# Optimization experiments

Hardware: AMD Instinct MI355X
Metric: run time of the kernel (lower is better)

## Reference

```python
import jax, jax.numpy as jnp
import numpy as np

B, N, D = 8, 256, 128


def setup_inputs() -> dict:
    key = jax.random.key(0)
    ks = jax.random.split(key, 4)
    s1 = 1.0 / np.sqrt(4 * D)
    s2 = 1.0 / np.sqrt(2 * D)
    s3 = 1.0 / np.sqrt(D)
    return {
        "tour_features": jax.random.normal(ks[0], (B, N, D), dtype=jnp.float32),
        "W1": jax.random.uniform(ks[1], (4 * D, 2 * D), jnp.float32, -s1, s1),
        "b1": jnp.zeros((2 * D,), jnp.float32),
        "W2": jax.random.uniform(ks[2], (2 * D, D), jnp.float32, -s2, s2),
        "b2": jnp.zeros((D,), jnp.float32),
        "W3": jax.random.uniform(ks[3], (D, 1), jnp.float32, -s3, s3),
        "b3": jnp.zeros((1,), jnp.float32),
    }


def reference(tour_features, W1, b1, W2, b2, W3, b3):
    Bs, Ns, Ds = tour_features.shape
    x = tour_features
    x_next = jnp.roll(x, -1, axis=1)  # node at (k+1) % N
    # Split first linear's weight by the 4 concatenated feature blocks:
    # cat([x_i, x_{i+1}, x_j, x_{j+1}]) @ W1 == x_i@W1a + x_{i+1}@W1b + x_j@W1c + x_{j+1}@W1d
    W1a, W1b, W1c, W1d = jnp.split(W1, 4, axis=0)
    Pi = x @ W1a + x_next @ W1b          # [B, N, 2D] (i-side projection)
    Pj = x @ W1c + x_next @ W1d          # [B, N, 2D] (j-side projection)
    h1 = jax.nn.relu(Pi[:, :, None, :] + Pj[:, None, :, :] + b1)  # [B, N, N, 2D]
    h2 = jax.nn.relu(h1 @ W2 + b2)       # [B, N, N, D]
    score = jnp.tanh((h2 @ W3 + b3)[..., 0])  # [B, N, N]
    # Valid pairs: j >= i + 2 and not (j - i == N - 1)
    ii = jnp.arange(Ns)[:, None]
    jj = jnp.arange(Ns)[None, :]
    mask = (jj >= ii + 2) & (jj - ii != Ns - 1)
    improvement_matrix = jnp.where(mask[None], score, 0.0)
    improved_tour = jnp.broadcast_to(jnp.arange(Ns), (Bs, Ns))
    return improved_tour, improvement_matrix
```

## Files before the change

### kernel.cpp

```cpp
#include <hip/hip_runtime.h>


typedef __attribute__((ext_vector_type(8))) short short8;
typedef __attribute__((ext_vector_type(8))) _Float16 half8;
typedef __attribute__((ext_vector_type(4))) float floatx4;

static __device__ __forceinline__ unsigned short f2bf(float f) {
  unsigned int x = __float_as_uint(f);
  x += 0x7fff + ((x >> 16) & 1);
  return (unsigned short)(x >> 16);
}

static __device__ __forceinline__ unsigned short f2h(float f) {
  _Float16 h = (_Float16)f;
  return __builtin_bit_cast(unsigned short, h);
}

static __device__ __forceinline__ float fast_tanh(float x) {
  float e = __expf(2.0f * fabsf(x));
  float t = 1.0f - 2.0f * __builtin_amdgcn_rcpf(e + 1.0f);
  return copysignf(t, x);
}

static __device__ __forceinline__ long pack_fp8(half8 s) {
  int lo = __builtin_amdgcn_cvt_pk_fp8_f32((float)s[0], (float)s[1], 0, false);
  lo = __builtin_amdgcn_cvt_pk_fp8_f32((float)s[2], (float)s[3], lo, true);
  int hi = __builtin_amdgcn_cvt_pk_fp8_f32((float)s[4], (float)s[5], 0, false);
  hi = __builtin_amdgcn_cvt_pk_fp8_f32((float)s[6], (float)s[7], hi, true);
  return (long)(unsigned)lo | ((long)hi << 32);
}

static __device__ __forceinline__ void gload_lds16(const void* g, void* l) {
  __builtin_amdgcn_global_load_lds(
      (const __attribute__((address_space(1))) unsigned int*)g,
      (__attribute__((address_space(3))) unsigned int*)l, 16, 0, 0);
}

__global__ __launch_bounds__(256) void k_prep(
    const float* __restrict__ x, const float* __restrict__ W1,
    const float* __restrict__ W2, float* __restrict__ out,
    unsigned char* __restrict__ W2F8, unsigned short* __restrict__ W1T,
    unsigned short* __restrict__ xcat) {
  int e = blockIdx.x * 256 + threadIdx.x;
  if (e < 2048) {
    out[e] = (float)(e & 255);
  } else if (e < 526336) {
    out[e] = 0.f;
  } else if (e < 542720) {
    int t = e - 526336;
    int p = t >> 7, n = t & 127;
    float f0 = W2[(2 * p) * 128 + n] * 16.f;
    float f1 = W2[(2 * p + 1) * 128 + n] * 16.f;
    int v2 = __builtin_amdgcn_cvt_pk_fp8_f32(f0, f1, 0, false);
    int q = n >> 5, which = (n >> 4) & 1, l = n & 15;
    int c = p >> 2, off = (p & 3) * 2;
    int cs = (c & 16) | ((c ^ l) & 15);
    *(unsigned short*)(W2F8 + q * 8192 + l * 512 + cs * 16 + which * 8 + off) =
        (unsigned short)(v2 & 0xffff);
  } else if (e < 673792) {
    int e3 = e - 542720;
    int n = e3 >> 8, k = e3 & 255;
    int v = k >> 3;
    int sw = (((v & 16) | ((v ^ (n & 15)) & 15)) << 3) | (k & 7);
    W1T[(n << 8) + sw] = f2bf(W1[((k + (n & 256)) << 8) + (n & 255)]);
  } else {
    int e4 = e - 673792;
    int r = e4 >> 8, k = e4 & 255;
    int v = k >> 3;
    int sw = (((v & 16) | ((v ^ (r & 15)) & 15)) << 3) | (k & 7);
    int pos = r & 255;
    int pos2 = (k < 128) ? pos : ((pos + 1) & 255);
    xcat[(r << 8) + sw] = f2bf(x[(((r >> 8) << 8) + pos2) * 128 + (k & 127)]);
  }
}

__global__ __launch_bounds__(256) void k_proj(
    const unsigned short* __restrict__ xcat, const unsigned short* __restrict__ W1T,
    const float* __restrict__ b1, unsigned short* __restrict__ PiH,
    unsigned short* __restrict__ PjH) {
  const int mg = blockIdx.x >> 3;
  const int ng = blockIdx.x & 7;
  const int tid = threadIdx.x;
  const int wr = tid >> 6, lane = tid & 63, quad = lane >> 4, l15 = lane & 15;

  __shared__ unsigned short As[64 * 256];
  __shared__ unsigned short Bs[64 * 256];

  const unsigned short* Asrc = xcat + mg * 64 * 256;
  const unsigned short* Bsrc = W1T + ng * 64 * 256;
#pragma unroll
  for (int it = 0; it < 8; ++it) {
    const int c = it * 256 + wr * 64 + lane;
    gload_lds16(Asrc + c * 8, &As[(it * 256 + wr * 64) * 8]);
    gload_lds16(Bsrc + c * 8, &Bs[(it * 256 + wr * 64) * 8]);
  }
  __syncthreads();

  floatx4 acc[4];
#pragma unroll
  for (int mt = 0; mt < 4; ++mt) acc[mt] = (floatx4)0.f;

  const char* Ab = (const char*)As;
  const char* Bb = (const char*)Bs + wr * 16 * 512;
  const int base_sw = l15 * 512 + ((quad ^ l15) << 4);

#pragma unroll
  for (int ks = 0; ks < 8; ++ks) {
    const int swz = base_sw ^ (ks << 6);
    short8 bfr = *(const short8*)(Bb + swz);
#pragma unroll
    for (int mt = 0; mt < 4; ++mt) {
      short8 afr = *(const short8*)(Ab + mt * 8192 + swz);
      acc[mt] = __builtin_amdgcn_mfma_f32_16x16x32_bf16(afr, bfr, acc[mt], 0, 0, 0);
    }
  }

  const int ch = ng * 64 + wr * 16 + l15;
  const float bias = (ch < 256) ? b1[ch] : 0.f;
  const bool isPi = (ch < 256);
  unsigned short* dst = isPi ? PiH : PjH;
  const int chan = ch & 255;
  const int ck = chan >> 3, coff = chan & 7;
#pragma unroll
  for (int mt = 0; mt < 4; ++mt)
#pragma unroll
    for (int r = 0; r < 4; ++r) {
      int row = mg * 64 + mt * 16 + quad * 4 + r;
      int cpos;
      if (isPi) cpos = chan;
      else {
        int cs = (ck & 16) | ((ck ^ (row & 15)) & 15);
        cpos = cs * 8 + coff;
      }
      dst[row * 256 + cpos] = f2h(acc[mt][r] + bias);
    }
}

__global__ __launch_bounds__(256, 3) void k_main(
    const unsigned short* __restrict__ PiH, const unsigned short* __restrict__ PjH,
    const unsigned char* __restrict__ W2F8, const float* __restrict__ b2,
    const float* __restrict__ W3, const float* __restrict__ b3,
    float* __restrict__ outm) {
  const int tid = threadIdx.x;
  const int wr = tid >> 6;
  const int lane = tid & 63, quad = lane >> 4, l15 = lane & 15;

  __shared__ unsigned char W2s[32768];
  __shared__ unsigned char PjS[16384];
  __shared__ unsigned char PiS[4096];

  const int bid = blockIdx.x;
  const int b = bid / 288;
  const int rem = bid - b * 288;
  int jt = 0, basej = 0;
  if (rem >= 8)   { jt = 1; basej = 8;   }
  if (rem >= 24)  { jt = 2; basej = 24;  }
  if (rem >= 48)  { jt = 3; basej = 48;  }
  if (rem >= 80)  { jt = 4; basej = 80;  }
  if (rem >= 120) { jt = 5; basej = 120; }
  if (rem >= 168) { jt = 6; basej = 168; }
  if (rem >= 224) { jt = 7; basej = 224; }
  const int i = (rem - basej) * 4 + wr;

  const unsigned char* pjsrc =
      (const unsigned char*)(PjH + ((b << 8) + jt * 32) * 256);
  const unsigned char* pisrc =
      (const unsigned char*)(PiH + ((b << 8) + i) * 256);
#pragma unroll
  for (int it = 0; it < 8; ++it) {
    const int c = it * 256 + wr * 64 + lane;
    gload_lds16(W2F8 + c * 16, &W2s[(it * 256 + wr * 64) * 16]);
  }
#pragma unroll
  for (int it = 0; it < 4; ++it) {
    const int c = it * 256 + wr * 64 + lane;
    gload_lds16(pjsrc + c * 16, &PjS[(it * 256 + wr * 64) * 16]);
  }
  gload_lds16(pisrc + (lane & 31) * 16, &PiS[wr * 1024]);
  __syncthreads();

  const char* W2base = (const char*)&W2s[0];
  const char* PjBase = (const char*)&PjS[0];
  const char* PiBase = (const char*)&PiS[0] + wr * 1024 + quad * 16;
  const int sw16 = l15 * 512 + (((quad ^ l15) & 15) << 4);

  floatx4 acc[2][8];
#pragma unroll
  for (int mt = 0; mt < 2; ++mt)
#pragma unroll
    for (int nt = 0; nt < 8; ++nt) acc[mt][nt] = (floatx4)0.f;

  union U4 { uint4 v; half8 h; };
  U4 piR[2], pjR[2][2];
  piR[0].v = *(const uint4*)(PiBase);
  pjR[0][0].v = *(const uint4*)(PjBase + sw16);
  pjR[0][1].v = *(const uint4*)(PjBase + 8192 + sw16);
  piR[1].v = *(const uint4*)(PiBase + 64);
  {
    const char* pj = PjBase + (sw16 ^ 64);
    pjR[1][0].v = *(const uint4*)(pj);
    pjR[1][1].v = *(const uint4*)(pj + 8192);
  }

  uint4 bfA[4], bfB[4];
  {
    const char* b0 = W2base + sw16;
#pragma unroll
    for (int q = 0; q < 4; ++q) bfA[q] = *(const uint4*)(b0 + q * 8192);
  }

  long aC0, aC1;
  {
    const half8 s0 = __builtin_elementwise_max(piR[0].h + pjR[0][0].h,
                                               (half8)(_Float16)0);
    const half8 s1 = __builtin_elementwise_max(piR[0].h + pjR[0][1].h,
                                               (half8)(_Float16)0);
    aC0 = pack_fp8(s0);
    aC1 = pack_fp8(s1);
  }

#pragma unroll
  for (int ks = 0; ks < 8; ++ks) {
    if (ks < 7) {
      const char* bn = W2base + (sw16 ^ ((ks + 1) << 6));
#pragma unroll
      for (int q = 0; q < 4; ++q)
        ((ks & 1) ? bfA : bfB)[q] = *(const uint4*)(bn + q * 8192);
    }
    if (ks < 6) {
      piR[ks & 1].v = *(const uint4*)(PiBase + (ks + 2) * 64);
      const char* pj = PjBase + (sw16 ^ ((ks + 2) << 6));
      pjR[ks & 1][0].v = *(const uint4*)(pj);
      pjR[ks & 1][1].v = *(const uint4*)(pj + 8192);
    }
    long aN0 = 0, aN1 = 0;
    if (ks < 7) {
      const half8 s0 = __builtin_elementwise_max(
          piR[(ks + 1) & 1].h + pjR[(ks + 1) & 1][0].h, (half8)(_Float16)0);
      const half8 s1 = __builtin_elementwise_max(
          piR[(ks + 1) & 1].h + pjR[(ks + 1) & 1][1].h, (half8)(_Float16)0);
      aN0 = pack_fp8(s0);
      aN1 = pack_fp8(s1);
    }
    const uint4* bc = (ks & 1) ? bfB : bfA;
    __builtin_amdgcn_s_setprio(1);
#pragma unroll
    for (int q = 0; q < 4; ++q) {
      const long blo = (long)bc[q].x | ((long)bc[q].y << 32);
      const long bhi = (long)bc[q].z | ((long)bc[q].w << 32);
      acc[0][2 * q]     = __builtin_amdgcn_mfma_f32_16x16x32_fp8_fp8(aC0, blo, acc[0][2 * q], 0, 0, 0);
      acc[1][2 * q]     = __builtin_amdgcn_mfma_f32_16x16x32_fp8_fp8(aC1, blo, acc[1][2 * q], 0, 0, 0);
      acc[0][2 * q + 1] = __builtin_amdgcn_mfma_f32_16x16x32_fp8_fp8(aC0, bhi, acc[0][2 * q + 1], 0, 0, 0);
      acc[1][2 * q + 1] = __builtin_amdgcn_mfma_f32_16x16x32_fp8_fp8(aC1, bhi, acc[1][2 * q + 1], 0, 0, 0);
    }
    __builtin_amdgcn_s_setprio(0);
    if (ks < 7) { aC0 = aN0; aC1 = aN1; }
  }

  float* orow = outm + ((b << 8) + i) * 256 + jt * 32;
  const float b3v = b3[0];
  const float s16 = 0.0625f;
#pragma unroll
  for (int mt = 0; mt < 2; ++mt) {
    float p0 = 0, p1 = 0, p2 = 0, p3 = 0;
#pragma unroll
    for (int nt = 0; nt < 8; ++nt) {
      float w3v = W3[nt * 16 + l15];
      float b2v = b2[nt * 16 + l15];
      floatx4 a = acc[mt][nt];
      p0 += fmaxf(fmaf(a[0], s16, b2v), 0.f) * w3v;
      p1 += fmaxf(fmaf(a[1], s16, b2v), 0.f) * w3v;
      p2 += fmaxf(fmaf(a[2], s16, b2v), 0.f) * w3v;
      p3 += fmaxf(fmaf(a[3], s16, b2v), 0.f) * w3v;
    }
#pragma unroll
    for (int m = 8; m >= 1; m >>= 1) {
      p0 += __shfl_xor(p0, m, 16);
      p1 += __shfl_xor(p1, m, 16);
      p2 += __shfl_xor(p2, m, 16);
      p3 += __shfl_xor(p3, m, 16);
    }
    if (l15 == 0) {
      const int jl = jt * 32 + mt * 16 + quad * 4;
      float ps[4] = {p0, p1, p2, p3};
#pragma unroll
      for (int r = 0; r < 4; ++r) {
        int j = jl + r;
        float sc = fast_tanh(ps[r] + b3v);
        bool valid = (j >= i + 2) && (j - i != 255);
        orow[mt * 16 + quad * 4 + r] = valid ? sc : 0.f;
      }
    }
  }
}

extern "C" void kernel_launch(void* const* d_in, const int* in_sizes, int n_in,
                              void* d_out, int out_size, void* d_ws, size_t ws_size,
                              hipStream_t stream) {
  const float* x  = (const float*)d_in[0];
  const float* W1 = (const float*)d_in[1];
  const float* b1 = (const float*)d_in[2];
  const float* W2 = (const float*)d_in[3];
  const float* b2 = (const float*)d_in[4];
  const float* W3 = (const float*)d_in[5];
  const float* b3 = (const float*)d_in[6];
  float* out = (float*)d_out;

  unsigned short* PiH  = (unsigned short*)d_ws;
  unsigned short* PjH  = PiH + 524288;
  unsigned short* W1T  = PjH + 524288;
  unsigned short* xcat = W1T + 131072;
  unsigned char*  W2F8 = (unsigned char*)(xcat + 524288);

  k_prep<<<4680, 256, 0, stream>>>(x, W1, W2, out, W2F8, W1T, xcat);
  k_proj<<<256, 256, 0, stream>>>(xcat, W1T, b1, PiH, PjH);
  k_main<<<2304, 256, 0, stream>>>(PiH, PjH, W2F8, b2, W3, b3, out + 2048);
}
```

Before: 97.27 us.

## Fuse x conversion into projection GEMM and move output/W2 prep into it

The separate xcat staging buffer is removed. The projection kernel now reads fp32 x directly, converts it to bf16 and writes it into swizzled LDS, which avoids a global write and re-read of the concatenated activations. Output initialization and the W2 fp8 packing move from the prep kernel into extra blocks of the projection kernel, and the output fill now uses vectorized stores. The prep kernel shrinks to only the W1 transpose, so less work sits serialized before the GEMM. In exchange, the A tile is loaded through registers instead of direct global-to-LDS loads.

```diff
diff --git a/kernel.cpp b/kernel.cpp
--- a/kernel.cpp
+++ b/kernel.cpp
@@ -37,62 +37,80 @@
 }
 
 __global__ __launch_bounds__(256) void k_prep(
-    const float* __restrict__ x, const float* __restrict__ W1,
-    const float* __restrict__ W2, float* __restrict__ out,
-    unsigned char* __restrict__ W2F8, unsigned short* __restrict__ W1T,
-    unsigned short* __restrict__ xcat) {
+    const float* __restrict__ W1, unsigned short* __restrict__ W1T) {
   int e = blockIdx.x * 256 + threadIdx.x;
-  if (e < 2048) {
-    out[e] = (float)(e & 255);
-  } else if (e < 526336) {
-    out[e] = 0.f;
-  } else if (e < 542720) {
-    int t = e - 526336;
-    int p = t >> 7, n = t & 127;
-    float f0 = W2[(2 * p) * 128 + n] * 16.f;
-    float f1 = W2[(2 * p + 1) * 128 + n] * 16.f;
-    int v2 = __builtin_amdgcn_cvt_pk_fp8_f32(f0, f1, 0, false);
-    int q = n >> 5, which = (n >> 4) & 1, l = n & 15;
-    int c = p >> 2, off = (p & 3) * 2;
-    int cs = (c & 16) | ((c ^ l) & 15);
-    *(unsigned short*)(W2F8 + q * 8192 + l * 512 + cs * 16 + which * 8 + off) =
-        (unsigned short)(v2 & 0xffff);
-  } else if (e < 673792) {
-    int e3 = e - 542720;
-    int n = e3 >> 8, k = e3 & 255;
-    int v = k >> 3;
-    int sw = (((v & 16) | ((v ^ (n & 15)) & 15)) << 3) | (k & 7);
-    W1T[(n << 8) + sw] = f2bf(W1[((k + (n & 256)) << 8) + (n & 255)]);
-  } else {
-    int e4 = e - 673792;
-    int r = e4 >> 8, k = e4 & 255;
-    int v = k >> 3;
-    int sw = (((v & 16) | ((v ^ (r & 15)) & 15)) << 3) | (k & 7);
-    int pos = r & 255;
-    int pos2 = (k < 128) ? pos : ((pos + 1) & 255);
-    xcat[(r << 8) + sw] = f2bf(x[(((r >> 8) << 8) + pos2) * 128 + (k & 127)]);
-  }
+  int n = e >> 8, k = e & 255;
+  int v = k >> 3;
+  int sw = (((v & 16) | ((v ^ (n & 15)) & 15)) << 3) | (k & 7);
+  W1T[(n << 8) + sw] = f2bf(W1[((k + (n & 256)) << 8) + (n & 255)]);
 }
 
 __global__ __launch_bounds__(256) void k_proj(
-    const unsigned short* __restrict__ xcat, const unsigned short* __restrict__ W1T,
+    const float* __restrict__ x, const unsigned short* __restrict__ W1T,
     const float* __restrict__ b1, unsigned short* __restrict__ PiH,
-    unsigned short* __restrict__ PjH) {
-  const int mg = blockIdx.x >> 3;
-  const int ng = blockIdx.x & 7;
+    unsigned short* __restrict__ PjH, const float* __restrict__ W2,
+    float* __restrict__ out, unsigned char* __restrict__ W2F8) {
   const int tid = threadIdx.x;
+  const int bx = blockIdx.x;
+
+  if (bx >= 256) {
+    if (bx < 770) {
+      int t = (bx - 256) * 256 + tid;
+      int e = t * 4;
+      floatx4 w;
+      if (e < 2048) {
+        float v = (float)(e & 255);
+        w = (floatx4){v, v + 1.f, v + 2.f, v + 3.f};
+      } else {
+        w = (floatx4)0.f;
+      }
+      *(floatx4*)(out + e) = w;
+    } else {
+      int t = (bx - 770) * 256 + tid;
+      int p = t >> 7, n = t & 127;
+      float f0 = W2[(2 * p) * 128 + n] * 16.f;
+      float f1 = W2[(2 * p + 1) * 128 + n] * 16.f;
+      int v2 = __builtin_amdgcn_cvt_pk_fp8_f32(f0, f1, 0, false);
+      int q = n >> 5, which = (n >> 4) & 1, l = n & 15;
+      int c = p >> 2, off = (p & 3) * 2;
+      int cs = (c & 16) | ((c ^ l) & 15);
+      *(unsigned short*)(W2F8 + q * 8192 + l * 512 + cs * 16 + which * 8 + off) =
+          (unsigned short)(v2 & 0xffff);
+    }
+    return;
+  }
+
+  const int mg = bx >> 3;
+  const int ng = bx & 7;
   const int wr = tid >> 6, lane = tid & 63, quad = lane >> 4, l15 = lane & 15;
 
   __shared__ unsigned short As[64 * 256];
   __shared__ unsigned short Bs[64 * 256];
 
-  const unsigned short* Asrc = xcat + mg * 64 * 256;
   const unsigned short* Bsrc = W1T + ng * 64 * 256;
 #pragma unroll
   for (int it = 0; it < 8; ++it) {
     const int c = it * 256 + wr * 64 + lane;
-    gload_lds16(Asrc + c * 8, &As[(it * 256 + wr * 64) * 8]);
     gload_lds16(Bsrc + c * 8, &Bs[(it * 256 + wr * 64) * 8]);
+  }
+
+#pragma unroll
+  for (int pass = 0; pass < 8; ++pass) {
+    const int rr = pass * 8 + (tid >> 5);
+    const int grow = mg * 64 + rr;
+    const int pos = grow & 255, bb = grow >> 8;
+    const int v = tid & 31;
+    const int pos2 = (v < 16) ? pos : ((pos + 1) & 255);
+    const float* src = x + (bb * 256 + pos2) * 128 + (v & 15) * 8;
+    const floatx4 f0 = *(const floatx4*)(src);
+    const floatx4 f1 = *(const floatx4*)(src + 4);
+    union { short8 s; unsigned short u[8]; } o;
+    o.u[0] = f2bf(f0[0]); o.u[1] = f2bf(f0[1]);
+    o.u[2] = f2bf(f0[2]); o.u[3] = f2bf(f0[3]);
+    o.u[4] = f2bf(f1[0]); o.u[5] = f2bf(f1[1]);
+    o.u[6] = f2bf(f1[2]); o.u[7] = f2bf(f1[3]);
+    const int sw = (v & 16) | ((v ^ (rr & 15)) & 15);
+    *(short8*)((char*)As + rr * 512 + sw * 16) = o.s;
   }
   __syncthreads();
 
@@ -309,10 +327,9 @@
   unsigned short* PiH  = (unsigned short*)d_ws;
   unsigned short* PjH  = PiH + 524288;
   unsigned short* W1T  = PjH + 524288;
-  unsigned short* xcat = W1T + 131072;
-  unsigned char*  W2F8 = (unsigned char*)(xcat + 524288);
-
-  k_prep<<<4680, 256, 0, stream>>>(x, W1, W2, out, W2F8, W1T, xcat);
-  k_proj<<<256, 256, 0, stream>>>(xcat, W1T, b1, PiH, PjH);
+  unsigned char*  W2F8 = (unsigned char*)(W1T + 131072);
+
+  k_prep<<<512, 256, 0, stream>>>(W1, W1T);
+  k_proj<<<834, 256, 0, stream>>>(x, W1T, b1, PiH, PjH, W2, out, W2F8);
   k_main<<<2304, 256, 0, stream>>>(PiH, PjH, W2F8, b2, W3, b3, out + 2048);
 }
```

Result: faster. 94.22 us (-3.1%).
